# Performance work log

Hardware: AMD Instinct MI355X
Metric: run time of the kernel (lower is better)

## Reference

```python
import jax, jax.numpy as jnp
import numpy as np
import math

B, SQ, SK, HEADS, DH = 4, 4096, 308, 8, 64
INNER = HEADS * DH


def setup_inputs() -> dict:
    key = jax.random.key(0)
    k1, k2, k3, k4, k5 = jax.random.split(key, 5)
    q = jax.random.normal(k1, (B, SQ, INNER), dtype=jnp.float32)
    k = jax.random.normal(k2, (B, SK, INNER), dtype=jnp.float32)
    v = jax.random.normal(k3, (B, SK, INNER), dtype=jnp.float32)
    # mask_scale: positive multiplicative rescale (H*W / mask_area in original)
    mask_scale = jax.random.uniform(k4, (B, HEADS, SQ, SK), dtype=jnp.float32) + 0.5
    # mask_bool: region membership mask (masks > 0.5 in original)
    mask_bool = jax.random.randint(k5, (B, HEADS, SQ, SK), 0, 2) > 0
    return {"q": q, "k": k, "v": v, "mask_scale": mask_scale,
            "mask_bool": mask_bool, "heads": HEADS}


def reference(q, k, v, mask_scale, mask_bool, heads):
    b, sq, inner = q.shape
    dh = inner // heads
    # (b, s, h*dh) -> (b, h, s, dh)
    def split_heads(t):
        return t.reshape(b, -1, heads, dh).transpose(0, 2, 1, 3)
    qh, kh, vh = split_heads(q), split_heads(k), split_heads(v)
    scores = jnp.einsum('bhqd,bhkd->bhqk', qh, kh) / math.sqrt(dh)
    scores = scores * mask_scale
    scores = jnp.where(mask_bool, scores, -jnp.inf)
    attn = jax.nn.softmax(scores, axis=-1)
    out = jnp.einsum('bhqk,bhkd->bhqd', attn, vh)
    # (b, h, q, dh) -> (b, q, h*dh)
    return out.transpose(0, 2, 1, 3).reshape(b, sq, heads * dh)
```

## Files before the change

### kernel.cpp

```cpp
#include <hip/hip_runtime.h>


#define NB     4
#define NSQ    4096
#define NSK    308
#define NH     8
#define NDH    64
#define NINNER 512
#define NKT    20
#define QBLK   64
#define NTHREADS 256
#define NCH    (QBLK*NSK/4)

#define KFRAG_PER_BH (NKT*2*64*8)
#define VFRAG_PER_BH (NKT*4*64*4)
#define WS_BYTES ((size_t)(NB*NH) * (KFRAG_PER_BH + VFRAG_PER_BH) * 2)

typedef _Float16 h8 __attribute__((ext_vector_type(8)));
typedef _Float16 h4 __attribute__((ext_vector_type(4)));
typedef float    f4 __attribute__((ext_vector_type(4)));
typedef int      i4 __attribute__((ext_vector_type(4)));

__global__ __launch_bounds__(512) void omost_prep(
    const float* __restrict__ Kg, const float* __restrict__ Vg,
    _Float16* __restrict__ ws)
{
  const int bh  = blockIdx.x;
  const int b   = bh >> 3;
  const int h   = bh & 7;
  const int tid = threadIdx.x;

  _Float16* Kfrag = ws + (size_t)bh * KFRAG_PER_BH;
  _Float16* Vfrag = ws + (size_t)(NB*NH) * KFRAG_PER_BH + (size_t)bh * VFRAG_PER_BH;

  const float* Kb = Kg + (size_t)b * NSK * NINNER + h * NDH;
  #pragma unroll
  for (int i = 0; i < (NKT*2*64) / 512; ++i) {
    int s   = tid + i * 512;
    int l   = s & 63;
    int dhc = (s >> 6) & 1;
    int kt  = s >> 7;
    int row = kt * 16 + (l & 15);
    int col = dhc * 32 + ((l >> 4) << 3);
    h8 hk;
    #pragma unroll
    for (int j = 0; j < 8; ++j) hk[j] = (_Float16)0.f;
    if (row < NSK) {
      const float* p = Kb + (size_t)row * NINNER + col;
      f4 a = *(const f4*)p;
      f4 c = *(const f4*)(p + 4);
      hk[0]=(_Float16)a[0]; hk[1]=(_Float16)a[1]; hk[2]=(_Float16)a[2]; hk[3]=(_Float16)a[3];
      hk[4]=(_Float16)c[0]; hk[5]=(_Float16)c[1]; hk[6]=(_Float16)c[2]; hk[7]=(_Float16)c[3];
    }
    *(h8*)(Kfrag + (size_t)s * 8) = hk;
  }

  const float* Vb = Vg + (size_t)b * NSK * NINNER + h * NDH;
  #pragma unroll
  for (int i = 0; i < (NKT*4*64) / 512; ++i) {
    int s    = tid + i * 512;
    int l    = s & 63;
    int nt   = (s >> 6) & 3;
    int kt   = s >> 8;
    int col  = nt * 16 + (l & 15);
    int row0 = kt * 16 + ((l >> 4) << 2);
    h4 hv;
    #pragma unroll
    for (int j = 0; j < 4; ++j) hv[j] = (_Float16)0.f;
    #pragma unroll
    for (int j = 0; j < 4; ++j) {
      int row = row0 + j;
      if (row < NSK) hv[j] = (_Float16)Vb[(size_t)row * NINNER + col];
    }
    *(h4*)(Vfrag + (size_t)s * 4) = hv;
  }
}

__global__ __launch_bounds__(NTHREADS) void omost_attn(
    const float* __restrict__ Qg, const float* __restrict__ MSg,
    const int*   __restrict__ MBg, const _Float16* __restrict__ ws,
    float* __restrict__ Og)
{
  __shared__ __align__(16) _Float16 Mlds[QBLK * NSK];

  const int tid  = threadIdx.x;
  const int lane = tid & 63;
  const int wv   = tid >> 6;
  const int lg   = lane >> 4;
  const int lr   = lane & 15;

  const int wg = blockIdx.x;
  const int qt = wg & (NSQ / QBLK - 1);
  const int bh = wg >> 6;
  const int b  = bh >> 3;
  const int h  = bh & 7;

  const int q0   = qt * QBLK + wv * 16;
  const int qrow = q0 + lr;

  const h8* Kf = (const h8*)(ws + (size_t)bh * KFRAG_PER_BH);
  const h4* Vf = (const h4*)(ws + (size_t)(NB*NH) * KFRAG_PER_BH + (size_t)bh * VFRAG_PER_BH);

  const float* Qb = Qg + ((size_t)b * NSQ + qrow) * NINNER + h * NDH;
  f4 qraw[4];
  qraw[0] = *(const f4*)(Qb + lg * 8);
  qraw[1] = *(const f4*)(Qb + lg * 8 + 4);
  qraw[2] = *(const f4*)(Qb + 32 + lg * 8);
  qraw[3] = *(const f4*)(Qb + 32 + lg * 8 + 4);

  const size_t mbase = ((size_t)bh * NSQ + qt * QBLK) * NSK;
  #pragma unroll
  for (int g = 0; g < 4; ++g) {
    f4 msr[5]; i4 mbr[5];
    #pragma unroll
    for (int j = 0; j < 5; ++j) {
      int cc  = tid + (g * 5 + j) * NTHREADS;
      int ccl = cc < NCH ? cc : NCH - 1;
      msr[j] = *(const f4*)(MSg + mbase + 4 * (size_t)ccl);
      mbr[j] = *(const i4*)(MBg + mbase + 4 * (size_t)ccl);
    }
    #pragma unroll
    for (int j = 0; j < 5; ++j) {
      int cc = tid + (g * 5 + j) * NTHREADS;
      if (cc < NCH) {
        h4 fm;
        #pragma unroll
        for (int r = 0; r < 4; ++r)
          fm[r] = (mbr[j][r] != 0) ? (_Float16)msr[j][r] : (_Float16)0.f;
        *(h4*)(&Mlds[4 * cc]) = fm;
      }
    }
  }
  __syncthreads();

  h8 qf0, qf1;
  {
    f4 a = qraw[0], c = qraw[1];
    qf0[0]=(_Float16)(a[0]*0.125f); qf0[1]=(_Float16)(a[1]*0.125f);
    qf0[2]=(_Float16)(a[2]*0.125f); qf0[3]=(_Float16)(a[3]*0.125f);
    qf0[4]=(_Float16)(c[0]*0.125f); qf0[5]=(_Float16)(c[1]*0.125f);
    qf0[6]=(_Float16)(c[2]*0.125f); qf0[7]=(_Float16)(c[3]*0.125f);
    a = qraw[2]; c = qraw[3];
    qf1[0]=(_Float16)(a[0]*0.125f); qf1[1]=(_Float16)(a[1]*0.125f);
    qf1[2]=(_Float16)(a[2]*0.125f); qf1[3]=(_Float16)(a[3]*0.125f);
    qf1[4]=(_Float16)(c[0]*0.125f); qf1[5]=(_Float16)(c[1]*0.125f);
    qf1[6]=(_Float16)(c[2]*0.125f); qf1[7]=(_Float16)(c[3]*0.125f);
  }

  const int mlrow = (wv * 16 + lr) * NSK;
  f4 acc0 = {0.f,0.f,0.f,0.f}, acc1 = {0.f,0.f,0.f,0.f};
  f4 acc2 = {0.f,0.f,0.f,0.f}, acc3 = {0.f,0.f,0.f,0.f};
  float ssum = 0.f;

#define MK_KBL(kt_) ((kt_) * 16 + lg * 4 > (NSK - 4) ? (NSK - 4) : (kt_) * 16 + lg * 4)

#define COMPUTE(kt_, k0_, k1_, v0_, v1_, v2_, v3_, m_)                           \
  do {                                                                           \
    const int kb_ = (kt_) * 16 + lg * 4;                                         \
    f4 c_ = {0.f, 0.f, 0.f, 0.f};                                                \
    c_ = __builtin_amdgcn_mfma_f32_16x16x32_f16((k0_), qf0, c_, 0, 0, 0);        \
    c_ = __builtin_amdgcn_mfma_f32_16x16x32_f16((k1_), qf1, c_, 0, 0, 0);        \
    h4 pa_;                                                                      \
    _Pragma("unroll")                                                            \
    for (int r = 0; r < 4; ++r) {                                                \
      float mf_ = (float)(m_)[r];                                                \
      bool ok_ = (kb_ + r < NSK) && (mf_ != 0.f);                                \
      float p_ = ok_ ? __expf(__builtin_fmaf(c_[r], mf_, -4.f)) : 0.f;           \
      ssum += p_;                                                                \
      pa_[r] = (_Float16)p_;                                                     \
    }                                                                            \
    acc0 = __builtin_amdgcn_mfma_f32_16x16x16f16(pa_, (v0_), acc0, 0, 0, 0);     \
    acc1 = __builtin_amdgcn_mfma_f32_16x16x16f16(pa_, (v1_), acc1, 0, 0, 0);     \
    acc2 = __builtin_amdgcn_mfma_f32_16x16x16f16(pa_, (v2_), acc2, 0, 0, 0);     \
    acc3 = __builtin_amdgcn_mfma_f32_16x16x16f16(pa_, (v3_), acc3, 0, 0, 0);     \
  } while (0)

  h8 kA0 = Kf[0 * 64 + lane], kA1 = Kf[1 * 64 + lane];
  h4 vA0 = Vf[0 * 64 + lane], vA1 = Vf[1 * 64 + lane];
  h4 vA2 = Vf[2 * 64 + lane], vA3 = Vf[3 * 64 + lane];
  h4 mA  = *(const h4*)(&Mlds[mlrow + MK_KBL(0)]);
  h8 kB0, kB1; h4 vB0, vB1, vB2, vB3, mB;

  #pragma unroll
  for (int p = 0; p < NKT / 2; ++p) {
    const int ktB = 2 * p + 1;
    kB0 = Kf[(ktB * 2 + 0) * 64 + lane];
    kB1 = Kf[(ktB * 2 + 1) * 64 + lane];
    vB0 = Vf[(ktB * 4 + 0) * 64 + lane];
    vB1 = Vf[(ktB * 4 + 1) * 64 + lane];
    vB2 = Vf[(ktB * 4 + 2) * 64 + lane];
    vB3 = Vf[(ktB * 4 + 3) * 64 + lane];
    mB  = *(const h4*)(&Mlds[mlrow + MK_KBL(ktB)]);
    COMPUTE(2 * p, kA0, kA1, vA0, vA1, vA2, vA3, mA);
    const int ktA = (2 * p + 2 < NKT) ? (2 * p + 2) : (NKT - 1);
    kA0 = Kf[(ktA * 2 + 0) * 64 + lane];
    kA1 = Kf[(ktA * 2 + 1) * 64 + lane];
    vA0 = Vf[(ktA * 4 + 0) * 64 + lane];
    vA1 = Vf[(ktA * 4 + 1) * 64 + lane];
    vA2 = Vf[(ktA * 4 + 2) * 64 + lane];
    vA3 = Vf[(ktA * 4 + 3) * 64 + lane];
    mA  = *(const h4*)(&Mlds[mlrow + MK_KBL(ktA)]);
    COMPUTE(2 * p + 1, kB0, kB1, vB0, vB1, vB2, vB3, mB);
  }
#undef COMPUTE
#undef MK_KBL

  ssum += __shfl_xor(ssum, 16, 64);
  ssum += __shfl_xor(ssum, 32, 64);
  const float inv = 1.f / fmaxf(ssum, 1e-30f);

  float invr[4];
  #pragma unroll
  for (int r = 0; r < 4; ++r) invr[r] = __shfl(inv, lg * 4 + r, 64);

  float* Ob = Og + (size_t)b * NSQ * NINNER + h * NDH;
  f4 accs[4] = {acc0, acc1, acc2, acc3};
  #pragma unroll
  for (int nt = 0; nt < 4; ++nt) {
    #pragma unroll
    for (int r = 0; r < 4; ++r) {
      int qq = q0 + lg * 4 + r;
      Ob[(size_t)qq * NINNER + nt * 16 + lr] = accs[nt][r] * invr[r];
    }
  }
}

extern "C" void kernel_launch(void* const* d_in, const int* in_sizes, int n_in,
                              void* d_out, int out_size, void* d_ws, size_t ws_size,
                              hipStream_t stream) {
  const float* Qg  = (const float*)d_in[0];
  const float* Kg  = (const float*)d_in[1];
  const float* Vg  = (const float*)d_in[2];
  const float* MSg = (const float*)d_in[3];
  const int*   MBg = (const int*)d_in[4];
  float* Og = (float*)d_out;
  _Float16* ws = (_Float16*)d_ws;

  if (ws_size < WS_BYTES) return;

  omost_prep<<<dim3(NB*NH), dim3(512), 0, stream>>>(Kg, Vg, ws);

  const int nwg = NB * NH * (NSQ / QBLK);
  omost_attn<<<dim3(nwg), dim3(NTHREADS), 0, stream>>>(Qg, MSg, MBg, ws, Og);
}
```

Before: 105.2 us.

## Halve query block to 32 rows with 128 threads and load mask lazily

Shrinks each workgroup from 64 query rows and 4 waves to 32 rows and 2 waves, doubling the grid and halving the LDS mask buffer per block, which should allow more resident blocks per CU. The mask staging loop now issues 10 loads per thread per group to keep the in-flight count. Mask values are read from LDS inside the compute step instead of being prefetched a tile ahead, which lowers register pressure. In exchange K/V fragments are re-read by twice as many blocks, and the LDS mask read is no longer overlapped with the preceding compute.

```diff
diff --git a/kernel.cpp b/kernel.cpp
--- a/kernel.cpp
+++ b/kernel.cpp
@@ -8,8 +8,8 @@
 #define NDH    64
 #define NINNER 512
 #define NKT    20
-#define QBLK   64
-#define NTHREADS 256
+#define QBLK   32
+#define NTHREADS 128
 #define NCH    (QBLK*NSK/4)
 
 #define KFRAG_PER_BH (NKT*2*64*8)
@@ -91,7 +91,7 @@
 
   const int wg = blockIdx.x;
   const int qt = wg & (NSQ / QBLK - 1);
-  const int bh = wg >> 6;
+  const int bh = wg >> 7;
   const int b  = bh >> 3;
   const int h  = bh & 7;
 
@@ -102,26 +102,25 @@
   const h4* Vf = (const h4*)(ws + (size_t)(NB*NH) * KFRAG_PER_BH + (size_t)bh * VFRAG_PER_BH);
 
   const float* Qb = Qg + ((size_t)b * NSQ + qrow) * NINNER + h * NDH;
-  f4 qraw[4];
-  qraw[0] = *(const f4*)(Qb + lg * 8);
-  qraw[1] = *(const f4*)(Qb + lg * 8 + 4);
-  qraw[2] = *(const f4*)(Qb + 32 + lg * 8);
-  qraw[3] = *(const f4*)(Qb + 32 + lg * 8 + 4);
+  f4 qraw0 = *(const f4*)(Qb + lg * 8);
+  f4 qraw1 = *(const f4*)(Qb + lg * 8 + 4);
+  f4 qraw2 = *(const f4*)(Qb + 32 + lg * 8);
+  f4 qraw3 = *(const f4*)(Qb + 32 + lg * 8 + 4);
 
   const size_t mbase = ((size_t)bh * NSQ + qt * QBLK) * NSK;
   #pragma unroll
-  for (int g = 0; g < 4; ++g) {
-    f4 msr[5]; i4 mbr[5];
-    #pragma unroll
-    for (int j = 0; j < 5; ++j) {
-      int cc  = tid + (g * 5 + j) * NTHREADS;
+  for (int g = 0; g < 2; ++g) {
+    f4 msr[10]; i4 mbr[10];
+    #pragma unroll
+    for (int j = 0; j < 10; ++j) {
+      int cc  = tid + (g * 10 + j) * NTHREADS;
       int ccl = cc < NCH ? cc : NCH - 1;
       msr[j] = *(const f4*)(MSg + mbase + 4 * (size_t)ccl);
       mbr[j] = *(const i4*)(MBg + mbase + 4 * (size_t)ccl);
     }
     #pragma unroll
-    for (int j = 0; j < 5; ++j) {
-      int cc = tid + (g * 5 + j) * NTHREADS;
+    for (int j = 0; j < 10; ++j) {
+      int cc = tid + (g * 10 + j) * NTHREADS;
       if (cc < NCH) {
         h4 fm;
         #pragma unroll
@@ -135,16 +134,14 @@
 
   h8 qf0, qf1;
   {
-    f4 a = qraw[0], c = qraw[1];
-    qf0[0]=(_Float16)(a[0]*0.125f); qf0[1]=(_Float16)(a[1]*0.125f);
-    qf0[2]=(_Float16)(a[2]*0.125f); qf0[3]=(_Float16)(a[3]*0.125f);
-    qf0[4]=(_Float16)(c[0]*0.125f); qf0[5]=(_Float16)(c[1]*0.125f);
-    qf0[6]=(_Float16)(c[2]*0.125f); qf0[7]=(_Float16)(c[3]*0.125f);
-    a = qraw[2]; c = qraw[3];
-    qf1[0]=(_Float16)(a[0]*0.125f); qf1[1]=(_Float16)(a[1]*0.125f);
-    qf1[2]=(_Float16)(a[2]*0.125f); qf1[3]=(_Float16)(a[3]*0.125f);
-    qf1[4]=(_Float16)(c[0]*0.125f); qf1[5]=(_Float16)(c[1]*0.125f);
-    qf1[6]=(_Float16)(c[2]*0.125f); qf1[7]=(_Float16)(c[3]*0.125f);
+    qf0[0]=(_Float16)(qraw0[0]*0.125f); qf0[1]=(_Float16)(qraw0[1]*0.125f);
+    qf0[2]=(_Float16)(qraw0[2]*0.125f); qf0[3]=(_Float16)(qraw0[3]*0.125f);
+    qf0[4]=(_Float16)(qraw1[0]*0.125f); qf0[5]=(_Float16)(qraw1[1]*0.125f);
+    qf0[6]=(_Float16)(qraw1[2]*0.125f); qf0[7]=(_Float16)(qraw1[3]*0.125f);
+    qf1[0]=(_Float16)(qraw2[0]*0.125f); qf1[1]=(_Float16)(qraw2[1]*0.125f);
+    qf1[2]=(_Float16)(qraw2[2]*0.125f); qf1[3]=(_Float16)(qraw2[3]*0.125f);
+    qf1[4]=(_Float16)(qraw3[0]*0.125f); qf1[5]=(_Float16)(qraw3[1]*0.125f);
+    qf1[6]=(_Float16)(qraw3[2]*0.125f); qf1[7]=(_Float16)(qraw3[3]*0.125f);
   }
 
   const int mlrow = (wv * 16 + lr) * NSK;
@@ -154,16 +151,17 @@
 
 #define MK_KBL(kt_) ((kt_) * 16 + lg * 4 > (NSK - 4) ? (NSK - 4) : (kt_) * 16 + lg * 4)
 
-#define COMPUTE(kt_, k0_, k1_, v0_, v1_, v2_, v3_, m_)                           \
+#define COMPUTE(kt_, k0_, k1_, v0_, v1_, v2_, v3_)                               \
   do {                                                                           \
     const int kb_ = (kt_) * 16 + lg * 4;                                         \
+    h4 m_ = *(const h4*)(&Mlds[mlrow + MK_KBL(kt_)]);                            \
     f4 c_ = {0.f, 0.f, 0.f, 0.f};                                                \
     c_ = __builtin_amdgcn_mfma_f32_16x16x32_f16((k0_), qf0, c_, 0, 0, 0);        \
     c_ = __builtin_amdgcn_mfma_f32_16x16x32_f16((k1_), qf1, c_, 0, 0, 0);        \
     h4 pa_;                                                                      \
     _Pragma("unroll")                                                            \
     for (int r = 0; r < 4; ++r) {                                                \
-      float mf_ = (float)(m_)[r];                                                \
+      float mf_ = (float)m_[r];                                                  \
       bool ok_ = (kb_ + r < NSK) && (mf_ != 0.f);                                \
       float p_ = ok_ ? __expf(__builtin_fmaf(c_[r], mf_, -4.f)) : 0.f;           \
       ssum += p_;                                                                \
@@ -178,8 +176,7 @@
   h8 kA0 = Kf[0 * 64 + lane], kA1 = Kf[1 * 64 + lane];
   h4 vA0 = Vf[0 * 64 + lane], vA1 = Vf[1 * 64 + lane];
   h4 vA2 = Vf[2 * 64 + lane], vA3 = Vf[3 * 64 + lane];
-  h4 mA  = *(const h4*)(&Mlds[mlrow + MK_KBL(0)]);
-  h8 kB0, kB1; h4 vB0, vB1, vB2, vB3, mB;
+  h8 kB0, kB1; h4 vB0, vB1, vB2, vB3;
 
   #pragma unroll
   for (int p = 0; p < NKT / 2; ++p) {
@@ -190,8 +187,7 @@
     vB1 = Vf[(ktB * 4 + 1) * 64 + lane];
     vB2 = Vf[(ktB * 4 + 2) * 64 + lane];
     vB3 = Vf[(ktB * 4 + 3) * 64 + lane];
-    mB  = *(const h4*)(&Mlds[mlrow + MK_KBL(ktB)]);
-    COMPUTE(2 * p, kA0, kA1, vA0, vA1, vA2, vA3, mA);
+    COMPUTE(2 * p, kA0, kA1, vA0, vA1, vA2, vA3);
     const int ktA = (2 * p + 2 < NKT) ? (2 * p + 2) : (NKT - 1);
     kA0 = Kf[(ktA * 2 + 0) * 64 + lane];
     kA1 = Kf[(ktA * 2 + 1) * 64 + lane];
@@ -199,8 +195,7 @@
     vA1 = Vf[(ktA * 4 + 1) * 64 + lane];
     vA2 = Vf[(ktA * 4 + 2) * 64 + lane];
     vA3 = Vf[(ktA * 4 + 3) * 64 + lane];
-    mA  = *(const h4*)(&Mlds[mlrow + MK_KBL(ktA)]);
-    COMPUTE(2 * p + 1, kB0, kB1, vB0, vB1, vB2, vB3, mB);
+    COMPUTE(2 * p + 1, kB0, kB1, vB0, vB1, vB2, vB3);
   }
 #undef COMPUTE
 #undef MK_KBL
```

Result: no change. 106.8 us (+1.6%).
